# Kernel optimization log

Measured on AMD Instinct MI355X. Metric: run time of the kernel, lower is better.

The kernel has to match this reference:

```python
import jax, jax.numpy as jnp
import numpy as np

D = 1024      # model_dim
H = 16        # num_heads
DH = D // H   # depth per head
F = 4096      # ffn_dim
B, L = 4, 2048
LN_EPS = 1e-5


def layer_norm(x, g, b):
    mu = jnp.mean(x, axis=-1, keepdims=True)
    var = jnp.var(x, axis=-1, keepdims=True)
    return (x - mu) * jax.lax.rsqrt(var + LN_EPS) * g + b


def setup_inputs() -> dict:
    key = jax.random.key(0)
    ks = jax.random.split(key, 12)
    s = 0.02
    return {
        "inputs": jax.random.normal(ks[0], (B, L, D), jnp.float32),
        "Wq": jax.random.normal(ks[1], (D, D), jnp.float32) * s,
        "Wk": jax.random.normal(ks[2], (D, D), jnp.float32) * s,
        "Wv": jax.random.normal(ks[3], (D, D), jnp.float32) * s,
        "Wo": jax.random.normal(ks[4], (D, D), jnp.float32) * s,
        "W1": jax.random.normal(ks[5], (F, D), jnp.float32) * s,
        "b1": jnp.zeros((F,), jnp.float32),
        "W2": jax.random.normal(ks[6], (D, F), jnp.float32) * s,
        "b2": jnp.zeros((D,), jnp.float32),
        "ln_g": jnp.ones((D,), jnp.float32),
        "ln_b": jnp.zeros((D,), jnp.float32),
    }


def reference(inputs, Wq, Wk, Wv, Wo, W1, b1, W2, b2, ln_g, ln_b):
    # --- MultiHeadAttention (faithful to source, incl. the bug where
    # ScaledDotProductAttention returns v, not attention @ v) ---
    scale = DH ** -0.5
    q = (inputs @ Wq.T) * scale            # [B,L,D], scaled before head split
    k = inputs @ Wk.T                      # [B,L,D]
    v = inputs @ Wv.T                      # [B,L,D]
    # only the LAST head's attention scores survive the python loop
    qH = q[..., (H - 1) * DH:]             # [B,L,DH]
    kH = k[..., (H - 1) * DH:]             # [B,L,DH]
    attn = jax.nn.softmax(jnp.einsum('bqd,bkd->bqk', qH, kH), axis=-1) / H
    # combine_heads(split_heads(v)) == v, so context = Wo applied to v
    context = v @ Wo.T                     # [B,L,D]; dropout(p=0) is identity

    # --- PositionalWiseFeedForward: conv1d(kernel=1) == pointwise linear ---
    h = jax.nn.relu(context @ W1.T + b1)   # [B,L,F]
    ffn = h @ W2.T + b2                    # [B,L,D]
    out = layer_norm(context + ffn, ln_g, ln_b)
    return out, attn
```

## Files before the change

kernel.cpp:

```cpp
#include <hip/hip_runtime.h>
#include <hip/hip_bf16.h>
#include <stdint.h>

#define D_ 1024
#define H_ 16
#define DH_ 64
#define F_ 4096
#define B_ 4
#define L_ 2048
#define MTOK 8192

typedef __attribute__((ext_vector_type(8))) short bf16x8;
typedef __attribute__((ext_vector_type(4))) float f32x4;

__device__ __forceinline__ short f2bf(float f) {
  uint32_t u = __float_as_uint(f);
  uint32_t r = (u + 0x7FFFu + ((u >> 16) & 1u)) >> 16;
  return (short)(uint16_t)r;
}
__device__ __forceinline__ float bf2f(short s) {
  return __uint_as_float(((uint32_t)(uint16_t)s) << 16);
}

__device__ __forceinline__ void gload_lds16(const short* g, short* l) {
  __builtin_amdgcn_global_load_lds(
      (const __attribute__((address_space(1))) void*)g,
      (__attribute__((address_space(3))) void*)l,
      16, 0, 0);
}

__global__ void __launch_bounds__(256) convert_bf16(
    const float* __restrict__ src, short* __restrict__ dst, long n, float scale) {
  long i = ((long)blockIdx.x * 256 + threadIdx.x) * 4;
  long stride = (long)gridDim.x * 1024;
  for (; i < n; i += stride) {
    float4 f = *(const float4*)(src + i);
    short4 o;
    o.x = f2bf(f.x * scale);
    o.y = f2bf(f.y * scale);
    o.z = f2bf(f.z * scale);
    o.w = f2bf(f.w * scale);
    *(short4*)(dst + i) = o;
  }
}

#define BAR   __builtin_amdgcn_s_barrier()
#define PRIO1 __builtin_amdgcn_s_setprio(1)
#define PRIO0 __builtin_amdgcn_s_setprio(0)
#define LGKM0 asm volatile("s_waitcnt lgkmcnt(0)" ::: "memory")

#define RD_A(mh_, par_) do {                                                  \
  const short* bp = lds + (par_) * BUF + wm * ASLOT;                          \
  _Pragma("unroll")                                                           \
  for (int m2 = 0; m2 < MH; m2++) {                                           \
    const int r = ((mh_) * MH + m2) * 16 + l15;                               \
    _Pragma("unroll")                                                         \
    for (int ks = 0; ks < 2; ks++)                                            \
      aF[mh_][m2][ks] =                                                       \
          *(const bf16x8*)(bp + r * 64 + (((ks * 4 + l4) ^ (r & 7)) << 3));   \
  } } while (0)

#define RD_B(nh_, par_) do {                                                  \
  const short* bp = lds + (par_) * BUF + BM * 64 + (wn >> 1) * 8192;          \
  _Pragma("unroll")                                                           \
  for (int n2 = 0; n2 < 2; n2++) {                                            \
    const int r = (wn & 1) * 64 + ((nh_) * 2 + n2) * 16 + l15;                \
    _Pragma("unroll")                                                         \
    for (int ks = 0; ks < 2; ks++)                                            \
      bF[nh_][n2][ks] =                                                       \
          *(const bf16x8*)(bp + r * 64 + (((ks * 4 + l4) ^ (r & 7)) << 3));   \
  } } while (0)

#define QUAD(mh_, nh_) do {                                                   \
  _Pragma("unroll")                                                           \
  for (int ks = 0; ks < 2; ks++)                                              \
    _Pragma("unroll")                                                         \
    for (int m2 = 0; m2 < MH; m2++)                                           \
      _Pragma("unroll")                                                       \
      for (int n2 = 0; n2 < 2; n2++)                                          \
        acc[(mh_) * MH + m2][(nh_) * 2 + n2] =                                \
            __builtin_amdgcn_mfma_f32_16x16x32_bf16(                          \
                aF[mh_][m2][ks], bF[nh_][n2][ks],                             \
                acc[(mh_) * MH + m2][(nh_) * 2 + n2], 0, 0, 0);               \
} while (0)

#define ITER2(g_, par_, SN, SPP, GK) do {                                     \
                                                                 \
  RD_A(0, par_); RD_B(0, par_); RD_B(1, par_);                                \
  if (SN) stA((g_) + 1, 1, (par_) ^ 1);                                       \
  LGKM0;                                                                      \
  PRIO1; QUAD(0, 0); QUAD(0, 1); PRIO0;                                       \
  BAR;              \
                                                                 \
  RD_A(1, par_);                                                              \
  if (SPP) { stB((g_) + 2, 0, par_); stB((g_) + 2, 1, par_);                  \
             stA((g_) + 2, 0, par_); }                                        \
  LGKM0;                                                                      \
  PRIO1; QUAD(1, 0); QUAD(1, 1); PRIO0;                                       \
  if (GK == 1) asm volatile("s_waitcnt vmcnt(%0)" :: "i"(VG) : "memory");     \
  else if (GK == 2) asm volatile("s_waitcnt vmcnt(0)" ::: "memory");          \
  BAR;                          \
} while (0)

template<int BMT, bool BIAS, bool RELU>
__global__ void __launch_bounds__(512, 2) gemm8p(
    const short* __restrict__ A, int lda,
    const short* __restrict__ Bm, int ldb,
    short* __restrict__ C, int ldc,
    const float* __restrict__ bias, int K) {
  constexpr int BM = BMT * 128;
  constexpr int MT = BMT * 4;
  constexpr int MH = MT / 2;
  constexpr int LA = BMT;
  constexpr int LB = 2;
  constexpr int ASLOT = (BM / 2) * 64;
  constexpr int BUF = BM * 64 + 16384;
  constexpr int VG = 2 * LB + LA;

  __shared__ __align__(16) short lds[2 * BUF];

  const int tid = threadIdx.x;
  const int lane = tid & 63;
  const int wave = tid >> 6;
  const int wm = wave >> 2, wn = wave & 3;
  const int l15 = lane & 15, l4 = lane >> 4;

  const int id = blockIdx.y * gridDim.x + blockIdx.x;
  const int per = (gridDim.x * gridDim.y) >> 3;
  const int swz = (id & 7) * per + (id >> 3);
  const int bn = swz % gridDim.x;
  const int bm = swz / gridDim.x;

  const short* Ab = A + (long)bm * BM * lda;
  const short* Bb = Bm + (long)bn * 256 * ldb;
  const int NTILE = K >> 6;

  const short* gA[2][LA]; short* dA[2][LA];
  const short* gB[2][LB]; short* dB[2][LB];
#pragma unroll
  for (int h = 0; h < 2; h++) {
#pragma unroll
    for (int l = 0; l < LA; l++) {
      int c = l * 512 + tid, r = c >> 3, cg = (c & 7) ^ (r & 7);
      gA[h][l] = Ab + (long)(h * (BM / 2) + r) * lda + cg * 8;
      dA[h][l] = lds + h * ASLOT + c * 8;
    }
#pragma unroll
    for (int l = 0; l < LB; l++) {
      int c = l * 512 + tid, r = c >> 3, cg = (c & 7) ^ (r & 7);
      gB[h][l] = Bb + (long)(h * 128 + r) * ldb + cg * 8;
      dB[h][l] = lds + BM * 64 + h * 8192 + c * 8;
    }
  }
  auto stA = [&](int t, int h, int par) {
#pragma unroll
    for (int l = 0; l < LA; l++)
      gload_lds16(gA[h][l] + (t << 6), dA[h][l] + par * BUF);
  };
  auto stB = [&](int t, int h, int par) {
#pragma unroll
    for (int l = 0; l < LB; l++)
      gload_lds16(gB[h][l] + (t << 6), dB[h][l] + par * BUF);
  };

  f32x4 acc[MT][4];
#pragma unroll
  for (int i = 0; i < MT; i++)
#pragma unroll
    for (int j = 0; j < 4; j++) acc[i][j] = (f32x4){0.f, 0.f, 0.f, 0.f};

  bf16x8 aF[2][MH][2];
  bf16x8 bF[2][2][2];

  stA(0, 0, 0); stA(0, 1, 0); stB(0, 0, 0); stB(0, 1, 0);
  stB(1, 0, 1); stB(1, 1, 1); stA(1, 0, 1);
  asm volatile("s_waitcnt vmcnt(%0)" :: "i"(VG) : "memory");
  BAR;

  for (int g = 0; g + 3 < NTILE; g += 2) {
    ITER2(g, 0, 1, 1, 1);
    ITER2(g + 1, 1, 1, 1, 1);
  }
  ITER2(NTILE - 2, 0, 1, 0, 2);
  ITER2(NTILE - 1, 1, 0, 0, 0);

  const int col0 = bn * 256 + wn * 64;
  const int row0 = bm * BM + wm * (BM / 2);
#pragma unroll
  for (int nt = 0; nt < 4; nt++) {
    const int col = col0 + nt * 16 + l15;
    const float bb = BIAS ? bias[col] : 0.f;
#pragma unroll
    for (int mt = 0; mt < MT; mt++) {
      const int rbase = row0 + mt * 16 + l4 * 4;
#pragma unroll
      for (int r = 0; r < 4; r++) {
        float v = acc[mt][nt][r] + bb;
        if (RELU) v = v > 0.f ? v : 0.f;
        C[(long)(rbase + r) * ldc + col] = f2bf(v);
      }
    }
  }
}

template<bool OUTF32>
__global__ void __launch_bounds__(256) gemm_bt(
    const short* __restrict__ A, int lda, long strideA,
    const short* __restrict__ Bm, int ldb, long strideB,
    void* __restrict__ Cv, int ldc, long strideC, int K) {
  const int bn = blockIdx.x;
  const int bm = blockIdx.y;
  const int bz = blockIdx.z;
  const short* Ab = A + (long)bz * strideA + (long)bm * 128 * lda;
  const short* Bb = Bm + (long)bz * strideB + (long)bn * 128 * ldb;

  __shared__ short lA[128 * 64];
  __shared__ short lB[128 * 64];

  const int tid = threadIdx.x;
  const int lane = tid & 63;
  const int wave = tid >> 6;
  const int wr = wave >> 1, wc = wave & 1;

  f32x4 acc[4][4];
#pragma unroll
  for (int i = 0; i < 4; i++)
#pragma unroll
    for (int j = 0; j < 4; j++) acc[i][j] = (f32x4){0.f, 0.f, 0.f, 0.f};

  for (int k0 = 0; k0 < K; k0 += 64) {
    __syncthreads();
#pragma unroll
    for (int i = 0; i < 4; i++) {
      int c = i * 256 + tid;
      int row = c >> 3;
      int col = (c & 7) * 8;
      gload_lds16(Ab + (long)row * lda + k0 + col, &lA[c * 8]);
      gload_lds16(Bb + (long)row * ldb + k0 + col, &lB[c * 8]);
    }
    __syncthreads();

#pragma unroll
    for (int ks = 0; ks < 2; ks++) {
      bf16x8 af[4], bfr[4];
#pragma unroll
      for (int t = 0; t < 4; t++) {
        af[t]  = *(const bf16x8*)&lA[(wr * 64 + t * 16 + (lane & 15)) * 64 + ks * 32 + (lane >> 4) * 8];
        bfr[t] = *(const bf16x8*)&lB[(wc * 64 + t * 16 + (lane & 15)) * 64 + ks * 32 + (lane >> 4) * 8];
      }
#pragma unroll
      for (int mt = 0; mt < 4; mt++)
#pragma unroll
        for (int nt = 0; nt < 4; nt++)
          acc[mt][nt] = __builtin_amdgcn_mfma_f32_16x16x32_bf16(af[mt], bfr[nt], acc[mt][nt], 0, 0, 0);
    }
  }

  const int col0 = bn * 128 + wc * 64;
  const int row0 = bm * 128 + wr * 64;
#pragma unroll
  for (int mt = 0; mt < 4; mt++) {
#pragma unroll
    for (int nt = 0; nt < 4; nt++) {
      int col = col0 + nt * 16 + (lane & 15);
      int rbase = row0 + mt * 16 + (lane >> 4) * 4;
#pragma unroll
      for (int r = 0; r < 4; r++) {
        float v = acc[mt][nt][r];
        long off = (long)bz * strideC + (long)(rbase + r) * ldc + col;
        if (OUTF32) ((float*)Cv)[off] = v;
        else        ((short*)Cv)[off] = f2bf(v);
      }
    }
  }
}

__device__ __forceinline__ float wave_sum(float v) {
#pragma unroll
  for (int o = 32; o > 0; o >>= 1) v += __shfl_xor(v, o, 64);
  return v;
}
__device__ __forceinline__ float wave_max(float v) {
#pragma unroll
  for (int o = 32; o > 0; o >>= 1) v = fmaxf(v, __shfl_xor(v, o, 64));
  return v;
}

__global__ void __launch_bounds__(256) softmax_div16(float* __restrict__ s) {
  const int tid = threadIdx.x;
  float* p = s + (long)blockIdx.x * 2048;
  float4 a = *(const float4*)(p + tid * 8);
  float4 b = *(const float4*)(p + tid * 8 + 4);
  float m = fmaxf(fmaxf(fmaxf(a.x, a.y), fmaxf(a.z, a.w)),
                  fmaxf(fmaxf(b.x, b.y), fmaxf(b.z, b.w)));
  __shared__ float red[4];
  m = wave_max(m);
  if ((tid & 63) == 0) red[tid >> 6] = m;
  __syncthreads();
  m = fmaxf(fmaxf(red[0], red[1]), fmaxf(red[2], red[3]));

  float e0 = __expf(a.x - m), e1 = __expf(a.y - m), e2 = __expf(a.z - m), e3 = __expf(a.w - m);
  float e4 = __expf(b.x - m), e5 = __expf(b.y - m), e6 = __expf(b.z - m), e7 = __expf(b.w - m);
  float sum = (e0 + e1) + (e2 + e3) + ((e4 + e5) + (e6 + e7));
  __syncthreads();
  sum = wave_sum(sum);
  if ((tid & 63) == 0) red[tid >> 6] = sum;
  __syncthreads();
  sum = red[0] + red[1] + red[2] + red[3];
  float inv = 1.0f / (sum * 16.0f);
  a.x = e0 * inv; a.y = e1 * inv; a.z = e2 * inv; a.w = e3 * inv;
  b.x = e4 * inv; b.y = e5 * inv; b.z = e6 * inv; b.w = e7 * inv;
  *(float4*)(p + tid * 8) = a;
  *(float4*)(p + tid * 8 + 4) = b;
}

__global__ void __launch_bounds__(256) ln_fuse(
    const short* __restrict__ ctx, const short* __restrict__ ffn,
    const float* __restrict__ g, const float* __restrict__ bta,
    float* __restrict__ out) {
  const int tid = threadIdx.x;
  long base = (long)blockIdx.x * 1024 + tid * 4;
  short4 c4 = *(const short4*)(ctx + base);
  short4 f4 = *(const short4*)(ffn + base);
  float x0 = bf2f(c4.x) + bf2f(f4.x);
  float x1 = bf2f(c4.y) + bf2f(f4.y);
  float x2 = bf2f(c4.z) + bf2f(f4.z);
  float x3 = bf2f(c4.w) + bf2f(f4.w);

  float s = (x0 + x1) + (x2 + x3);
  float q = (x0 * x0 + x1 * x1) + (x2 * x2 + x3 * x3);
  __shared__ float rs[4], rq[4];
  s = wave_sum(s);
  q = wave_sum(q);
  if ((tid & 63) == 0) { rs[tid >> 6] = s; rq[tid >> 6] = q; }
  __syncthreads();
  float S = rs[0] + rs[1] + rs[2] + rs[3];
  float Q = rq[0] + rq[1] + rq[2] + rq[3];
  float mu = S * (1.0f / 1024.0f);
  float var = Q * (1.0f / 1024.0f) - mu * mu;
  float inv = rsqrtf(var + 1e-5f);

  float4 g4 = *(const float4*)(g + tid * 4);
  float4 b4 = *(const float4*)(bta + tid * 4);
  float4 o;
  o.x = (x0 - mu) * inv * g4.x + b4.x;
  o.y = (x1 - mu) * inv * g4.y + b4.y;
  o.z = (x2 - mu) * inv * g4.z + b4.z;
  o.w = (x3 - mu) * inv * g4.w + b4.w;
  *(float4*)(out + base) = o;
}

extern "C" void kernel_launch(void* const* d_in, const int* in_sizes, int n_in,
                              void* d_out, int out_size, void* d_ws, size_t ws_size,
                              hipStream_t stream) {
  const float* inputs = (const float*)d_in[0];
  const float* Wq = (const float*)d_in[1];
  const float* Wk = (const float*)d_in[2];
  const float* Wv = (const float*)d_in[3];
  const float* Wo = (const float*)d_in[4];
  const float* W1 = (const float*)d_in[5];
  const float* b1 = (const float*)d_in[6];
  const float* W2 = (const float*)d_in[7];
  const float* b2 = (const float*)d_in[8];
  const float* ln_g = (const float*)d_in[9];
  const float* ln_b = (const float*)d_in[10];

  char* w = (char*)d_ws;
  short* in_bf = (short*)w;  w += (long)MTOK * D_ * 2;
  short* wqk   = (short*)w;  w += 128L * D_ * 2;
  short* wv    = (short*)w;  w += (long)D_ * D_ * 2;
  short* wo    = (short*)w;  w += (long)D_ * D_ * 2;
  short* w1    = (short*)w;  w += (long)F_ * D_ * 2;
  short* w2    = (short*)w;  w += (long)D_ * F_ * 2;
  short* qkh   = (short*)w;  w += (long)MTOK * 128 * 2;
  short* vbf   = (short*)w;  w += (long)MTOK * D_ * 2;
  short* ctxbf = (short*)w;  w += (long)MTOK * D_ * 2;
  short* hbf   = (short*)w;  w += (long)MTOK * F_ * 2;
  short* ffnbf = (short*)w;  w += (long)MTOK * D_ * 2;

  float* out  = (float*)d_out;
  float* attn = out + (long)MTOK * D_;

  const float scale = 0.125f;

  convert_bf16<<<dim3((MTOK * D_) >> 10), 256, 0, stream>>>(inputs, in_bf, (long)MTOK * D_, 1.0f);
  convert_bf16<<<dim3((64 * D_) >> 10), 256, 0, stream>>>(Wq + 960 * D_, wqk, 64L * D_, scale);
  convert_bf16<<<dim3((64 * D_) >> 10), 256, 0, stream>>>(Wk + 960 * D_, wqk + 64L * D_, 64L * D_, 1.0f);
  convert_bf16<<<dim3((D_ * D_) >> 10), 256, 0, stream>>>(Wv, wv, (long)D_ * D_, 1.0f);
  convert_bf16<<<dim3((D_ * D_) >> 10), 256, 0, stream>>>(Wo, wo, (long)D_ * D_, 1.0f);
  convert_bf16<<<dim3((F_ * D_) >> 10), 256, 0, stream>>>(W1, w1, (long)F_ * D_, 1.0f);
  convert_bf16<<<dim3((F_ * D_) >> 10), 256, 0, stream>>>(W2, w2, (long)F_ * D_, 1.0f);

  gemm_bt<false><<<dim3(1, 64, 1), 256, 0, stream>>>(
      in_bf, D_, 0, wqk, D_, 0, qkh, 128, 0, D_);
  gemm8p<1, false, false><<<dim3(4, 64), 512, 0, stream>>>(
      in_bf, D_, wv, D_, vbf, D_, nullptr, D_);
  gemm_bt<true><<<dim3(16, 16, 4), 256, 0, stream>>>(
      qkh, 128, (long)L_ * 128, qkh + 64, 128, (long)L_ * 128,
      attn, L_, (long)L_ * L_, 64);
  softmax_div16<<<dim3(MTOK), 256, 0, stream>>>(attn);
  gemm8p<1, false, false><<<dim3(4, 64), 512, 0, stream>>>(
      vbf, D_, wo, D_, ctxbf, D_, nullptr, D_);
  gemm8p<2, true, true><<<dim3(16, 32), 512, 0, stream>>>(
      ctxbf, D_, w1, D_, hbf, F_, b1, D_);
  gemm8p<1, true, false><<<dim3(4, 64), 512, 0, stream>>>(
      hbf, F_, w2, F_, ffnbf, D_, b2, F_);
  ln_fuse<<<dim3(MTOK), 256, 0, stream>>>(ctxbf, ffnbf, ln_g, ln_b, out);
}
```

Measured before the change: 289.6 us.

## Fuse QK^T scores with softmax and merge weight conversions into one launch

```diff
diff --git a/kernel.cpp b/kernel.cpp
--- a/kernel.cpp
+++ b/kernel.cpp
@@ -42,6 +42,27 @@
     o.w = f2bf(f.w * scale);
     *(short4*)(dst + i) = o;
   }
+}
+
+__global__ void __launch_bounds__(256) convert_weights(
+    const float* __restrict__ Wq, const float* __restrict__ Wk,
+    const float* __restrict__ Wv, const float* __restrict__ Wo,
+    const float* __restrict__ W1, const float* __restrict__ W2,
+    short* __restrict__ wqk, short* __restrict__ wv, short* __restrict__ wo,
+    short* __restrict__ w1, short* __restrict__ w2) {
+  long i = ((long)blockIdx.x * 256 + threadIdx.x) * 4;
+  const float* src; short* dst; long off; float scale = 1.0f;
+  if (i < 65536L)            { src = Wq + 960L * 1024; dst = wqk;        off = i;            scale = 0.125f; }
+  else if (i < 131072L)      { src = Wk + 960L * 1024; dst = wqk + 65536; off = i - 65536L;  }
+  else if (i < 1179648L)     { src = Wv; dst = wv; off = i - 131072L;   }
+  else if (i < 2228224L)     { src = Wo; dst = wo; off = i - 1179648L;  }
+  else if (i < 6422528L)     { src = W1; dst = w1; off = i - 2228224L;  }
+  else                       { src = W2; dst = w2; off = i - 6422528L;  }
+  float4 f = *(const float4*)(src + off);
+  short4 o4;
+  o4.x = f2bf(f.x * scale); o4.y = f2bf(f.y * scale);
+  o4.z = f2bf(f.z * scale); o4.w = f2bf(f.w * scale);
+  *(short4*)(dst + off) = o4;
 }
 
 #define BAR   __builtin_amdgcn_s_barrier()
@@ -203,16 +224,14 @@
   }
 }
 
-template<bool OUTF32>
 __global__ void __launch_bounds__(256) gemm_bt(
-    const short* __restrict__ A, int lda, long strideA,
-    const short* __restrict__ Bm, int ldb, long strideB,
-    void* __restrict__ Cv, int ldc, long strideC, int K) {
+    const short* __restrict__ A, int lda,
+    const short* __restrict__ Bm, int ldb,
+    short* __restrict__ C, int ldc, int K) {
   const int bn = blockIdx.x;
   const int bm = blockIdx.y;
-  const int bz = blockIdx.z;
-  const short* Ab = A + (long)bz * strideA + (long)bm * 128 * lda;
-  const short* Bb = Bm + (long)bz * strideB + (long)bn * 128 * ldb;
+  const short* Ab = A + (long)bm * 128 * lda;
+  const short* Bb = Bm + (long)bn * 128 * ldb;
 
   __shared__ short lA[128 * 64];
   __shared__ short lB[128 * 64];
@@ -265,12 +284,80 @@
       int col = col0 + nt * 16 + (lane & 15);
       int rbase = row0 + mt * 16 + (lane >> 4) * 4;
 #pragma unroll
-      for (int r = 0; r < 4; r++) {
-        float v = acc[mt][nt][r];
-        long off = (long)bz * strideC + (long)(rbase + r) * ldc + col;
-        if (OUTF32) ((float*)Cv)[off] = v;
-        else        ((short*)Cv)[off] = f2bf(v);
-      }
+      for (int r = 0; r < 4; r++)
+        C[(long)(rbase + r) * ldc + col] = f2bf(acc[mt][nt][r]);
+    }
+  }
+}
+
+__global__ void __launch_bounds__(256) fused_attn(
+    const short* __restrict__ qkh, float* __restrict__ attn) {
+  const int tid = threadIdx.x;
+  const int lane = tid & 63;
+  const int wave = tid >> 6;
+  const int grp = wave >> 1;
+  const int half = wave & 1;
+  const int l15 = lane & 15, l4 = lane >> 4;
+  const int b = blockIdx.y;
+  const int q0 = blockIdx.x * 32 + grp * 16;
+  const long base = (long)b * 2048;
+
+  bf16x8 qf[2];
+#pragma unroll
+  for (int ks = 0; ks < 2; ks++)
+    qf[ks] = *(const bf16x8*)&qkh[(base + q0 + l15) * 128 + ks * 32 + l4 * 8];
+
+  const short* kb = qkh + (base + (long)half * 1024) * 128 + 64;
+
+  float m = -1e30f, s = 0.f;
+  for (int kt = 0; kt < 64; kt++) {
+    bf16x8 kf0 = *(const bf16x8*)&kb[(kt * 16 + l15) * 128 + l4 * 8];
+    bf16x8 kf1 = *(const bf16x8*)&kb[(kt * 16 + l15) * 128 + 32 + l4 * 8];
+    f32x4 acc = (f32x4){0.f, 0.f, 0.f, 0.f};
+    acc = __builtin_amdgcn_mfma_f32_16x16x32_bf16(kf0, qf[0], acc, 0, 0, 0);
+    acc = __builtin_amdgcn_mfma_f32_16x16x32_bf16(kf1, qf[1], acc, 0, 0, 0);
+    float pm = fmaxf(fmaxf(acc[0], acc[1]), fmaxf(acc[2], acc[3]));
+    float mn = fmaxf(m, pm);
+    s = s * __expf(m - mn) + __expf(acc[0] - mn) + __expf(acc[1] - mn) +
+        __expf(acc[2] - mn) + __expf(acc[3] - mn);
+    m = mn;
+  }
+#pragma unroll
+  for (int o = 16; o <= 32; o <<= 1) {
+    float m2 = __shfl_xor(m, o, 64);
+    float s2 = __shfl_xor(s, o, 64);
+    float mn = fmaxf(m, m2);
+    s = s * __expf(m - mn) + s2 * __expf(m2 - mn);
+    m = mn;
+  }
+  __shared__ float lm[2][2][16], lsm[2][2][16];
+  if (lane < 16) { lm[grp][half][lane] = m; lsm[grp][half][lane] = s; }
+  __syncthreads();
+  {
+    float m0 = lm[grp][0][l15], m1 = lm[grp][1][l15];
+    float s0 = lsm[grp][0][l15], s1 = lsm[grp][1][l15];
+    float M = fmaxf(m0, m1);
+    s = s0 * __expf(m0 - M) + s1 * __expf(m1 - M);
+    m = M;
+  }
+  const float inv = 1.0f / (s * 16.0f);
+
+  __shared__ float tb[4][256];
+  float* attb = attn + (base + q0) * 2048 + half * 1024;
+  for (int kt = 0; kt < 64; kt++) {
+    bf16x8 kf0 = *(const bf16x8*)&kb[(kt * 16 + l15) * 128 + l4 * 8];
+    bf16x8 kf1 = *(const bf16x8*)&kb[(kt * 16 + l15) * 128 + 32 + l4 * 8];
+    f32x4 acc = (f32x4){0.f, 0.f, 0.f, 0.f};
+    acc = __builtin_amdgcn_mfma_f32_16x16x32_bf16(kf0, qf[0], acc, 0, 0, 0);
+    acc = __builtin_amdgcn_mfma_f32_16x16x32_bf16(kf1, qf[1], acc, 0, 0, 0);
+    f32x4 p;
+#pragma unroll
+    for (int r = 0; r < 4; r++) p[r] = __expf(acc[r] - m) * inv;
+    *(f32x4*)&tb[wave][l15 * 16 + l4 * 4] = p;
+#pragma unroll
+    for (int rr = 0; rr < 4; rr++) {
+      int row = rr * 4 + l4;
+      attb[(long)row * 2048 + kt * 16 + l15] = tb[wave][row * 16 + l15];
     }
   }
 }
@@ -279,39 +366,6 @@
 #pragma unroll
   for (int o = 32; o > 0; o >>= 1) v += __shfl_xor(v, o, 64);
   return v;
-}
-__device__ __forceinline__ float wave_max(float v) {
-#pragma unroll
-  for (int o = 32; o > 0; o >>= 1) v = fmaxf(v, __shfl_xor(v, o, 64));
-  return v;
-}
-
-__global__ void __launch_bounds__(256) softmax_div16(float* __restrict__ s) {
-  const int tid = threadIdx.x;
-  float* p = s + (long)blockIdx.x * 2048;
-  float4 a = *(const float4*)(p + tid * 8);
-  float4 b = *(const float4*)(p + tid * 8 + 4);
-  float m = fmaxf(fmaxf(fmaxf(a.x, a.y), fmaxf(a.z, a.w)),
-                  fmaxf(fmaxf(b.x, b.y), fmaxf(b.z, b.w)));
-  __shared__ float red[4];
-  m = wave_max(m);
-  if ((tid & 63) == 0) red[tid >> 6] = m;
-  __syncthreads();
-  m = fmaxf(fmaxf(red[0], red[1]), fmaxf(red[2], red[3]));
-
-  float e0 = __expf(a.x - m), e1 = __expf(a.y - m), e2 = __expf(a.z - m), e3 = __expf(a.w - m);
-  float e4 = __expf(b.x - m), e5 = __expf(b.y - m), e6 = __expf(b.z - m), e7 = __expf(b.w - m);
-  float sum = (e0 + e1) + (e2 + e3) + ((e4 + e5) + (e6 + e7));
-  __syncthreads();
-  sum = wave_sum(sum);
-  if ((tid & 63) == 0) red[tid >> 6] = sum;
-  __syncthreads();
-  sum = red[0] + red[1] + red[2] + red[3];
-  float inv = 1.0f / (sum * 16.0f);
-  a.x = e0 * inv; a.y = e1 * inv; a.z = e2 * inv; a.w = e3 * inv;
-  b.x = e4 * inv; b.y = e5 * inv; b.z = e6 * inv; b.w = e7 * inv;
-  *(float4*)(p + tid * 8) = a;
-  *(float4*)(p + tid * 8 + 4) = b;
 }
 
 __global__ void __launch_bounds__(256) ln_fuse(
@@ -381,24 +435,15 @@
   float* out  = (float*)d_out;
   float* attn = out + (long)MTOK * D_;
 
-  const float scale = 0.125f;
-
-  convert_bf16<<<dim3((MTOK * D_) >> 10), 256, 0, stream>>>(inputs, in_bf, (long)MTOK * D_, 1.0f);
-  convert_bf16<<<dim3((64 * D_) >> 10), 256, 0, stream>>>(Wq + 960 * D_, wqk, 64L * D_, scale);
-  convert_bf16<<<dim3((64 * D_) >> 10), 256, 0, stream>>>(Wk + 960 * D_, wqk + 64L * D_, 64L * D_, 1.0f);
-  convert_bf16<<<dim3((D_ * D_) >> 10), 256, 0, stream>>>(Wv, wv, (long)D_ * D_, 1.0f);
-  convert_bf16<<<dim3((D_ * D_) >> 10), 256, 0, stream>>>(Wo, wo, (long)D_ * D_, 1.0f);
-  convert_bf16<<<dim3((F_ * D_) >> 10), 256, 0, stream>>>(W1, w1, (long)F_ * D_, 1.0f);
-  convert_bf16<<<dim3((F_ * D_) >> 10), 256, 0, stream>>>(W2, w2, (long)F_ * D_, 1.0f);
-
-  gemm_bt<false><<<dim3(1, 64, 1), 256, 0, stream>>>(
-      in_bf, D_, 0, wqk, D_, 0, qkh, 128, 0, D_);
+  convert_bf16<<<dim3((MTOK * D_) >> 10), 256, 0, stream>>>(
+      inputs, in_bf, (long)MTOK * D_, 1.0f);
+  convert_weights<<<dim3(10368), 256, 0, stream>>>(
+      Wq, Wk, Wv, Wo, W1, W2, wqk, wv, wo, w1, w2);
+
+  gemm_bt<<<dim3(1, 64), 256, 0, stream>>>(in_bf, D_, wqk, D_, qkh, 128, D_);
+  fused_attn<<<dim3(64, 4), 256, 0, stream>>>(qkh, attn);
   gemm8p<1, false, false><<<dim3(4, 64), 512, 0, stream>>>(
       in_bf, D_, wv, D_, vbf, D_, nullptr, D_);
-  gemm_bt<true><<<dim3(16, 16, 4), 256, 0, stream>>>(
-      qkh, 128, (long)L_ * 128, qkh + 64, 128, (long)L_ * 128,
-      attn, L_, (long)L_ * L_, 64);
-  softmax_div16<<<dim3(MTOK), 256, 0, stream>>>(attn);
   gemm8p<1, false, false><<<dim3(4, 64), 512, 0, stream>>>(
       vbf, D_, wo, D_, ctxbf, D_, nullptr, D_);
   gemm8p<2, true, true><<<dim3(16, 32), 512, 0, stream>>>(
```

Measured after the change: 298.1 us. 2.9% more time.
